# Performance work log

Hardware: AMD Instinct MI355X
Metric: run time of the kernel (lower is better)

The kernel has to match this reference:

```python
import jax, jax.numpy as jnp
import numpy as np

NUM_BOXES = 512
NUM_COORDS = 200000
C = 128
MAX_SELECTED = 262144  # static pad size for the ragged output
P_INSIDE = 0.002       # expected ~204.8k selected rows < MAX_SELECTED


def setup_inputs() -> dict:
    key = jax.random.key(0)
    k1, k2, k3 = jax.random.split(key, 3)
    coords = jax.random.randint(k1, (NUM_COORDS, 4), 0, 256, dtype=jnp.int32)
    features = jax.random.normal(k2, (NUM_COORDS, C), dtype=jnp.float32)
    is_inside = jax.random.uniform(k3, (NUM_BOXES, NUM_COORDS)) < P_INSIDE
    return {"coords": coords, "features": features, "is_inside": is_inside,
            "max_selected": MAX_SELECTED}


def reference(coords, features, is_inside, max_selected):
    # Faithful to select_coords/select_features, but WITHOUT materializing the
    # dense (num_boxes, num_coords, C) expand: compute flat nonzero indices of
    # the mask directly and gather once. Output is padded to a static size
    # (padded rows zeroed) since jax requires static shapes.
    num_boxes, num_coords = is_inside.shape
    total = num_boxes * num_coords
    flat_idx = jnp.nonzero(is_inside.ravel(), size=max_selected, fill_value=total)[0]
    valid = flat_idx < total                      # [K] pad mask
    safe = jnp.where(valid, flat_idx, 0)
    box_idx = (safe // num_coords).astype(jnp.int32)   # [K]
    coord_idx = safe % num_coords                       # [K]
    # select_features: features[None].expand(...)[is_inside]
    selected_features = jnp.where(valid[:, None], features[coord_idx], 0.0)  # [K, C]
    # select_coords: cat(coords[:, :-1] gathered, box index)
    sel_xyz = coords[coord_idx, :-1]                    # [K, 3]
    ext_coords = jnp.concatenate([sel_xyz, box_idx[:, None]], axis=-1)  # [K, 4]
    extended_coordinates = jnp.where(valid[:, None], ext_coords, 0)
    return extended_coordinates, selected_features
```

## Files before the change

### kernel.cpp

```cpp
#include <hip/hip_runtime.h>


#define NB 2048
#define BS 256

__device__ __forceinline__ int cb4(unsigned w){
  return (int)((w & 0x000000ffu)!=0) + (int)((w & 0x0000ff00u)!=0) +
         (int)((w & 0x00ff0000u)!=0) + (int)((w & 0xff000000u)!=0);
}

__global__ void init_flag(int* flag){ *flag = 0; }

__global__ void detect_mode(const uchar4* p, int nvec, int* flag){
  int found = 0;
  for (int i = blockIdx.x*blockDim.x + threadIdx.x; i < nvec;
       i += gridDim.x*blockDim.x){
    uchar4 v = p[i];
    if (v.y) found = 1;
  }
  if (found) atomicOr(flag, 1);
}

__global__ void count_kernel(const uint4* data, const int* flag,
                             long long totalElems, int epb, int* counts){
  const bool byteMode = (*flag != 0);
  const int tid = threadIdx.x;
  const long long elemBase = (long long)blockIdx.x * (long long)epb;
  int cnt = 0;
  if (byteMode){
    const int nvec = epb >> 4;
    const uint4* base = data + (elemBase >> 4);
    for (int v = tid; v < nvec; v += BS){
      if (elemBase + ((long long)v << 4) >= totalElems) break;
      uint4 x = base[v];
      cnt += cb4(x.x)+cb4(x.y)+cb4(x.z)+cb4(x.w);
    }
  } else {
    const int nvec = epb >> 2;
    const uint4* base = data + (elemBase >> 2);
    for (int v = tid; v < nvec; v += BS){
      if (elemBase + ((long long)v << 2) >= totalElems) break;
      uint4 x = base[v];
      cnt += (int)(x.x!=0)+(int)(x.y!=0)+(int)(x.z!=0)+(int)(x.w!=0);
    }
  }
  const int lane = tid & 63, wid = tid >> 6;
  for (int off = 32; off > 0; off >>= 1) cnt += __shfl_down(cnt, off, 64);
  __shared__ int wsum[BS/64];
  if (lane == 0) wsum[wid] = cnt;
  __syncthreads();
  if (tid == 0){
    int s = 0;
    for (int w = 0; w < BS/64; ++w) s += wsum[w];
    counts[blockIdx.x] = s;
  }
}

__global__ void scan_kernel(const int* counts, int* offsets, int* totalOut, int nb){
  const int tid = threadIdx.x;
  const int per = (nb + BS - 1)/BS;
  const int base = tid*per;
  int vals[16];
  int sum = 0;
  for (int k = 0; k < per; ++k){
    int idx = base + k;
    int c = (idx < nb) ? counts[idx] : 0;
    vals[k] = sum; sum += c;
  }
  int incl = sum;
  const int lane = tid & 63, wid = tid >> 6;
  for (int off = 1; off < 64; off <<= 1){
    int t = __shfl_up(incl, off, 64);
    if (lane >= off) incl += t;
  }
  __shared__ int wsum[BS/64];
  if (lane == 63) wsum[wid] = incl;
  __syncthreads();
  int wbase = 0;
  for (int w = 0; w < wid; ++w) wbase += wsum[w];
  const int excl = wbase + incl - sum;
  for (int k = 0; k < per; ++k){
    int idx = base + k;
    if (idx < nb) offsets[idx] = excl + vals[k];
  }
  if (tid == BS-1){
    int t = 0;
    for (int w = 0; w < BS/64; ++w) t += wsum[w];
    *totalOut = t;
  }
}

__global__ void compact_kernel(const uint4* data, const int* flag, const int* offsets,
                               long long totalElems, int epb, int max_sel, int* outIdx){
  const bool byteMode = (*flag != 0);
  const int tid = threadIdx.x;
  const int lane = tid & 63, wid = tid >> 6;
  const long long elemBase = (long long)blockIdx.x * (long long)epb;
  int running = offsets[blockIdx.x];
  __shared__ int wsum[BS/64];

  if (byteMode){
    const int nvec = epb >> 4;
    const uint4* base = data + (elemBase >> 4);
    const int iters = (nvec + BS - 1)/BS;
    for (int it = 0; it < iters; ++it){
      const int v = it*BS + tid;
      uint4 x = make_uint4(0u,0u,0u,0u);
      const bool active = (v < nvec) &&
                          (elemBase + ((long long)v << 4) < totalElems);
      if (active) x = base[v];
      const int cnt = cb4(x.x)+cb4(x.y)+cb4(x.z)+cb4(x.w);
      int incl = cnt;
      for (int off = 1; off < 64; off <<= 1){
        int t = __shfl_up(incl, off, 64);
        if (lane >= off) incl += t;
      }
      if (lane == 63) wsum[wid] = incl;
      __syncthreads();
      int wbase = 0;
      for (int w = 0; w < wid; ++w) wbase += wsum[w];
      int iterTotal = 0;
      for (int w = 0; w < BS/64; ++w) iterTotal += wsum[w];
      int pos = running + wbase + incl - cnt;
      if (cnt){
        const long long e0 = elemBase + ((long long)v << 4);
        unsigned words[4] = {x.x, x.y, x.z, x.w};
        #pragma unroll
        for (int wI = 0; wI < 4; ++wI){
          unsigned w = words[wI];
          #pragma unroll
          for (int b = 0; b < 4; ++b){
            if ((w >> (8*b)) & 0xffu){
              if (pos < max_sel) outIdx[pos] = (int)(e0 + wI*4 + b);
              ++pos;
            }
          }
        }
      }
      running += iterTotal;
      __syncthreads();
    }
  } else {
    const int nvec = epb >> 2;
    const uint4* base = data + (elemBase >> 2);
    const int iters = (nvec + BS - 1)/BS;
    for (int it = 0; it < iters; ++it){
      const int v = it*BS + tid;
      uint4 x = make_uint4(0u,0u,0u,0u);
      const bool active = (v < nvec) &&
                          (elemBase + ((long long)v << 2) < totalElems);
      if (active) x = base[v];
      const int cnt = (int)(x.x!=0)+(int)(x.y!=0)+(int)(x.z!=0)+(int)(x.w!=0);
      int incl = cnt;
      for (int off = 1; off < 64; off <<= 1){
        int t = __shfl_up(incl, off, 64);
        if (lane >= off) incl += t;
      }
      if (lane == 63) wsum[wid] = incl;
      __syncthreads();
      int wbase = 0;
      for (int w = 0; w < wid; ++w) wbase += wsum[w];
      int iterTotal = 0;
      for (int w = 0; w < BS/64; ++w) iterTotal += wsum[w];
      int pos = running + wbase + incl - cnt;
      if (cnt){
        const long long e0 = elemBase + ((long long)v << 2);
        unsigned words[4] = {x.x, x.y, x.z, x.w};
        #pragma unroll
        for (int j = 0; j < 4; ++j){
          if (words[j]){
            if (pos < max_sel) outIdx[pos] = (int)(e0 + j);
            ++pos;
          }
        }
      }
      running += iterTotal;
      __syncthreads();
    }
  }
}

__global__ void gather_kernel(const int* selIdx, const int* totalPtr,
                              const int4* coords, const float4* feat,
                              int num_coords, int c4, int max_sel,
                              float4* outExt, float4* outFeat){
  const int lane = threadIdx.x & 31;
  const int rowsPerBlock = blockDim.x >> 5;
  const int r = blockIdx.x*rowsPerBlock + (threadIdx.x >> 5);
  if (r >= max_sel) return;
  int total = *totalPtr;
  if (total > max_sel) total = max_sel;
  if (r < total){
    const int flat = selIdx[r];
    const unsigned box = (unsigned)flat / (unsigned)num_coords;
    const int ci = flat - (int)box*num_coords;
    const float4* src = feat + (long long)ci*c4;
    float4* dst = outFeat + (long long)r*c4;
    for (int c = lane; c < c4; c += 32) dst[c] = src[c];
    if (lane == 0){
      int4 cc = coords[ci];
      outExt[r] = make_float4((float)cc.x, (float)cc.y, (float)cc.z, (float)box);
    }
  } else {
    const float4 z = make_float4(0.f, 0.f, 0.f, 0.f);
    float4* dst = outFeat + (long long)r*c4;
    for (int c = lane; c < c4; c += 32) dst[c] = z;
    if (lane == 0) outExt[r] = z;
  }
}

extern "C" void kernel_launch(void* const* d_in, const int* in_sizes, int n_in,
                              void* d_out, int out_size, void* d_ws, size_t ws_size,
                              hipStream_t stream){
  const int*   coords   = (const int*)d_in[0];
  const float* features = (const float*)d_in[1];
  const void*  inside   = d_in[2];

  const int num_coords = in_sizes[0] / 4;
  const int C          = in_sizes[1] / num_coords;
  const int c4         = C / 4;
  const long long totalElems = (long long)in_sizes[2];
  const int max_sel    = out_size / (4 + C);

  int* ws      = (int*)d_ws;
  int* flag    = ws;
  int* total   = ws + 1;
  int* counts  = ws + 2;
  int* offsets = ws + 2 + NB;
  int* selIdx  = ws + 2 + 2*NB;

  int epb = (int)((totalElems + NB - 1) / NB);
  epb = (epb + 15) & ~15;

  hipLaunchKernelGGL(init_flag, dim3(1), dim3(1), 0, stream, flag);
  hipLaunchKernelGGL(detect_mode, dim3(32), dim3(BS), 0, stream,
                     (const uchar4*)inside, 65536 , flag);
  hipLaunchKernelGGL(count_kernel, dim3(NB), dim3(BS), 0, stream,
                     (const uint4*)inside, flag, totalElems, epb, counts);
  hipLaunchKernelGGL(scan_kernel, dim3(1), dim3(BS), 0, stream,
                     counts, offsets, total, NB);
  hipLaunchKernelGGL(compact_kernel, dim3(NB), dim3(BS), 0, stream,
                     (const uint4*)inside, flag, offsets, totalElems, epb,
                     max_sel, selIdx);
  const int rowsPerBlock = BS / 32;
  const int gblocks = (max_sel + rowsPerBlock - 1) / rowsPerBlock;
  hipLaunchKernelGGL(gather_kernel, dim3(gblocks), dim3(BS), 0, stream,
                     selIdx, total, (const int4*)coords, (const float4*)features,
                     num_coords, c4, max_sel,
                     (float4*)d_out,
                     (float4*)((float*)d_out + (long long)max_sel*4));
}
```

Measured before the change: 740.1 us.

## Pack inside-mask into bitmask during counting and emit indices from bitmask

The count pass now turns each 32 mask elements into a 32-bit bitmask word, using a SWAR byte-nonzero trick in byte mode, and stores it in workspace. The compaction pass then reads this compact bitmask instead of re-reading the full mask, and emits indices with find-first-set loops. This removes a second full read of the ~100 MB mask. The flag init kernel is also dropped in favour of per-block detection flags. It costs an extra write and read of a small bitmask buffer and changes the per-block partitioning, so the number of blocks scanned grows to about three thousand.

```diff
diff --git a/kernel.cpp b/kernel.cpp
--- a/kernel.cpp
+++ b/kernel.cpp
@@ -1,47 +1,87 @@
 #include <hip/hip_runtime.h>
 
 
-#define NB 2048
-#define BS 256
-
-__device__ __forceinline__ int cb4(unsigned w){
-  return (int)((w & 0x000000ffu)!=0) + (int)((w & 0x0000ff00u)!=0) +
-         (int)((w & 0x00ff0000u)!=0) + (int)((w & 0xff000000u)!=0);
-}
-
-__global__ void init_flag(int* flag){ *flag = 0; }
-
-__global__ void detect_mode(const uchar4* p, int nvec, int* flag){
+#define BS  256
+#define WPB 1024
+#define DETB 32
+
+__device__ __forceinline__ unsigned nzmask4(unsigned v){
+  unsigned t = (v | ((v & 0x7f7f7f7fu) + 0x7f7f7f7fu)) & 0x80808080u;
+  return ((t >> 7) & 1u) | ((t >> 14) & 2u) | ((t >> 21) & 4u) | ((t >> 28) & 8u);
+}
+__device__ __forceinline__ unsigned nzmask16(uint4 x){
+  return nzmask4(x.x) | (nzmask4(x.y) << 4) | (nzmask4(x.z) << 8) | (nzmask4(x.w) << 12);
+}
+
+__global__ void detect_mode(const uchar4* p, int nvec, int* flags){
   int found = 0;
   for (int i = blockIdx.x*blockDim.x + threadIdx.x; i < nvec;
        i += gridDim.x*blockDim.x){
     uchar4 v = p[i];
     if (v.y) found = 1;
   }
-  if (found) atomicOr(flag, 1);
-}
-
-__global__ void count_kernel(const uint4* data, const int* flag,
-                             long long totalElems, int epb, int* counts){
-  const bool byteMode = (*flag != 0);
+  __shared__ int sh;
+  if (threadIdx.x == 0) sh = 0;
+  __syncthreads();
+  if (found) atomicOr(&sh, 1);
+  __syncthreads();
+  if (threadIdx.x == 0) flags[blockIdx.x] = sh;
+}
+
+__global__ void pack_count(const void* data, const int* flags,
+                           long long totalElems, int wordsTotal,
+                           unsigned* maskOut, int* counts){
+  __shared__ int modeSh;
+  if (threadIdx.x == 0){
+    int f = 0;
+    for (int i = 0; i < DETB; ++i) f |= flags[i];
+    modeSh = f;
+  }
+  __syncthreads();
+  const bool byteMode = (modeSh != 0);
   const int tid = threadIdx.x;
-  const long long elemBase = (long long)blockIdx.x * (long long)epb;
   int cnt = 0;
+  const int wBase = blockIdx.x * WPB;
   if (byteMode){
-    const int nvec = epb >> 4;
-    const uint4* base = data + (elemBase >> 4);
-    for (int v = tid; v < nvec; v += BS){
-      if (elemBase + ((long long)v << 4) >= totalElems) break;
-      uint4 x = base[v];
-      cnt += cb4(x.x)+cb4(x.y)+cb4(x.z)+cb4(x.w);
+    const uint4* d = (const uint4*)data;
+    const unsigned char* p8 = (const unsigned char*)data;
+    for (int i = tid; i < WPB; i += BS){
+      const int w = wBase + i;
+      if (w >= wordsTotal) break;
+      const long long e0 = (long long)w << 5;
+      unsigned m;
+      if (e0 + 31 < totalElems){
+        uint4 a = d[2*w], b = d[2*w+1];
+        m = nzmask16(a) | (nzmask16(b) << 16);
+      } else {
+        m = 0;
+        for (int b = 0; b < 32 && e0 + b < totalElems; ++b)
+          if (p8[e0 + b]) m |= (1u << b);
+      }
+      maskOut[w] = m;
+      cnt += __popc(m);
     }
   } else {
-    const int nvec = epb >> 2;
-    const uint4* base = data + (elemBase >> 2);
-    for (int v = tid; v < nvec; v += BS){
-      if (elemBase + ((long long)v << 2) >= totalElems) break;
-      uint4 x = base[v];
-      cnt += (int)(x.x!=0)+(int)(x.y!=0)+(int)(x.z!=0)+(int)(x.w!=0);
+    const uint4* d = (const uint4*)data;
+    const unsigned* p32 = (const unsigned*)data;
+    for (int i = tid; i < WPB; i += BS){
+      const int w = wBase + i;
+      if (w >= wordsTotal) break;
+      const long long e0 = (long long)w << 5;
+      unsigned m = 0;
+      if (e0 + 31 < totalElems){
+        #pragma unroll
+        for (int k = 0; k < 8; ++k){
+          uint4 x = d[8*(long long)w + k];
+          m |= ((unsigned)(x.x!=0) << (4*k)) | ((unsigned)(x.y!=0) << (4*k+1)) |
+               ((unsigned)(x.z!=0) << (4*k+2)) | ((unsigned)(x.w!=0) << (4*k+3));
+        }
+      } else {
+        for (int b = 0; b < 32 && e0 + b < totalElems; ++b)
+          if (p32[e0 + b]) m |= (1u << b);
+      }
+      maskOut[w] = m;
+      cnt += __popc(m);
     }
   }
   const int lane = tid & 63, wid = tid >> 6;
@@ -90,93 +130,42 @@
   }
 }
 
-__global__ void compact_kernel(const uint4* data, const int* flag, const int* offsets,
-                               long long totalElems, int epb, int max_sel, int* outIdx){
-  const bool byteMode = (*flag != 0);
+__global__ void emit_kernel(const unsigned* mask, const int* offsets,
+                            int wordsTotal, int max_sel, int* outIdx){
   const int tid = threadIdx.x;
   const int lane = tid & 63, wid = tid >> 6;
-  const long long elemBase = (long long)blockIdx.x * (long long)epb;
+  const int wBase = blockIdx.x * WPB;
   int running = offsets[blockIdx.x];
   __shared__ int wsum[BS/64];
-
-  if (byteMode){
-    const int nvec = epb >> 4;
-    const uint4* base = data + (elemBase >> 4);
-    const int iters = (nvec + BS - 1)/BS;
-    for (int it = 0; it < iters; ++it){
-      const int v = it*BS + tid;
-      uint4 x = make_uint4(0u,0u,0u,0u);
-      const bool active = (v < nvec) &&
-                          (elemBase + ((long long)v << 4) < totalElems);
-      if (active) x = base[v];
-      const int cnt = cb4(x.x)+cb4(x.y)+cb4(x.z)+cb4(x.w);
-      int incl = cnt;
-      for (int off = 1; off < 64; off <<= 1){
-        int t = __shfl_up(incl, off, 64);
-        if (lane >= off) incl += t;
+  const int iters = WPB / BS;
+  for (int it = 0; it < iters; ++it){
+    const int w = wBase + it*BS + tid;
+    unsigned m = (w < wordsTotal) ? mask[w] : 0u;
+    const int cnt = __popc(m);
+    int incl = cnt;
+    for (int off = 1; off < 64; off <<= 1){
+      int t = __shfl_up(incl, off, 64);
+      if (lane >= off) incl += t;
+    }
+    if (lane == 63) wsum[wid] = incl;
+    __syncthreads();
+    int wbase = 0;
+    for (int ww = 0; ww < wid; ++ww) wbase += wsum[ww];
+    int iterTotal = 0;
+    for (int ww = 0; ww < BS/64; ++ww) iterTotal += wsum[ww];
+    int pos = running + wbase + incl - cnt;
+    if (m){
+      const long long e0 = (long long)w << 5;
+      unsigned mm = m;
+      while (mm){
+        const int b = __ffs(mm) - 1;
+        mm &= mm - 1;
+        if (pos < max_sel) outIdx[pos] = (int)(e0 + b);
+        ++pos;
       }
-      if (lane == 63) wsum[wid] = incl;
-      __syncthreads();
-      int wbase = 0;
-      for (int w = 0; w < wid; ++w) wbase += wsum[w];
-      int iterTotal = 0;
-      for (int w = 0; w < BS/64; ++w) iterTotal += wsum[w];
-      int pos = running + wbase + incl - cnt;
-      if (cnt){
-        const long long e0 = elemBase + ((long long)v << 4);
-        unsigned words[4] = {x.x, x.y, x.z, x.w};
-        #pragma unroll
-        for (int wI = 0; wI < 4; ++wI){
-          unsigned w = words[wI];
-          #pragma unroll
-          for (int b = 0; b < 4; ++b){
-            if ((w >> (8*b)) & 0xffu){
-              if (pos < max_sel) outIdx[pos] = (int)(e0 + wI*4 + b);
-              ++pos;
-            }
-          }
-        }
-      }
-      running += iterTotal;
-      __syncthreads();
-    }
-  } else {
-    const int nvec = epb >> 2;
-    const uint4* base = data + (elemBase >> 2);
-    const int iters = (nvec + BS - 1)/BS;
-    for (int it = 0; it < iters; ++it){
-      const int v = it*BS + tid;
-      uint4 x = make_uint4(0u,0u,0u,0u);
-      const bool active = (v < nvec) &&
-                          (elemBase + ((long long)v << 2) < totalElems);
-      if (active) x = base[v];
-      const int cnt = (int)(x.x!=0)+(int)(x.y!=0)+(int)(x.z!=0)+(int)(x.w!=0);
-      int incl = cnt;
-      for (int off = 1; off < 64; off <<= 1){
-        int t = __shfl_up(incl, off, 64);
-        if (lane >= off) incl += t;
-      }
-      if (lane == 63) wsum[wid] = incl;
-      __syncthreads();
-      int wbase = 0;
-      for (int w = 0; w < wid; ++w) wbase += wsum[w];
-      int iterTotal = 0;
-      for (int w = 0; w < BS/64; ++w) iterTotal += wsum[w];
-      int pos = running + wbase + incl - cnt;
-      if (cnt){
-        const long long e0 = elemBase + ((long long)v << 2);
-        unsigned words[4] = {x.x, x.y, x.z, x.w};
-        #pragma unroll
-        for (int j = 0; j < 4; ++j){
-          if (words[j]){
-            if (pos < max_sel) outIdx[pos] = (int)(e0 + j);
-            ++pos;
-          }
-        }
-      }
-      running += iterTotal;
-      __syncthreads();
-    }
+    }
+    running += iterTotal;
+    __syncthreads();
   }
 }
 
@@ -222,26 +211,25 @@
   const long long totalElems = (long long)in_sizes[2];
   const int max_sel    = out_size / (4 + C);
 
+  const int wordsTotal = (int)((totalElems + 31) / 32);
+  const int NBP        = (wordsTotal + WPB - 1) / WPB;
+
   int* ws      = (int*)d_ws;
-  int* flag    = ws;
-  int* total   = ws + 1;
-  int* counts  = ws + 2;
-  int* offsets = ws + 2 + NB;
-  int* selIdx  = ws + 2 + 2*NB;
-
-  int epb = (int)((totalElems + NB - 1) / NB);
-  epb = (epb + 15) & ~15;
-
-  hipLaunchKernelGGL(init_flag, dim3(1), dim3(1), 0, stream, flag);
-  hipLaunchKernelGGL(detect_mode, dim3(32), dim3(BS), 0, stream,
-                     (const uchar4*)inside, 65536 , flag);
-  hipLaunchKernelGGL(count_kernel, dim3(NB), dim3(BS), 0, stream,
-                     (const uint4*)inside, flag, totalElems, epb, counts);
+  int* flags   = ws;
+  int* total   = ws + DETB;
+  int* counts  = ws + DETB + 1;
+  int* offsets = counts + NBP;
+  int* selIdx  = offsets + NBP;
+  unsigned* maskBuf = (unsigned*)(selIdx + max_sel);
+
+  hipLaunchKernelGGL(detect_mode, dim3(DETB), dim3(BS), 0, stream,
+                     (const uchar4*)inside, 65536 , flags);
+  hipLaunchKernelGGL(pack_count, dim3(NBP), dim3(BS), 0, stream,
+                     inside, flags, totalElems, wordsTotal, maskBuf, counts);
   hipLaunchKernelGGL(scan_kernel, dim3(1), dim3(BS), 0, stream,
-                     counts, offsets, total, NB);
-  hipLaunchKernelGGL(compact_kernel, dim3(NB), dim3(BS), 0, stream,
-                     (const uint4*)inside, flag, offsets, totalElems, epb,
-                     max_sel, selIdx);
+                     counts, offsets, total, NBP);
+  hipLaunchKernelGGL(emit_kernel, dim3(NBP), dim3(BS), 0, stream,
+                     maskBuf, offsets, wordsTotal, max_sel, selIdx);
   const int rowsPerBlock = BS / 32;
   const int gblocks = (max_sel + rowsPerBlock - 1) / rowsPerBlock;
   hipLaunchKernelGGL(gather_kernel, dim3(gblocks), dim3(BS), 0, stream,
```

After: 670.9 us, median of 2. 9.4% less time.
